# Kernel tuning notes

Hardware: AMD Instinct MI355X
Metric: run time of the kernel (lower is better)

## Reference

```python
import jax, jax.numpy as jnp
import numpy as np

D_MODEL, D_HIDDEN = 1024, 2048
B, L = 4, 4096


def setup_inputs() -> dict:
    key = jax.random.key(0)
    ks = jax.random.split(key, 16)
    r = lambda k, shape, s: s * jax.random.normal(k, shape, dtype=jnp.float32)
    inp = {
        "x": r(ks[0], (B, L, D_MODEL), 1.0),
        # MambaBlock weights (torch Linear stores [out, in]; bias=False for these)
        "w1": r(ks[1], (D_MODEL, D_MODEL), 0.02),
        "w2": r(ks[2], (D_MODEL, D_MODEL), 0.02),
        "w3": r(ks[3], (D_MODEL, D_MODEL), 0.02),
        # depthwise Conv1d: weight [D, 1, 3], bias [D]
        "conv_w": r(ks[4], (D_MODEL, 1, 3), 0.1),
        "conv_b": r(ks[5], (D_MODEL,), 0.02),
        # SSM linears (with bias). Scales keep exp(-delta*A) in (0,1) and
        # the length-L cumprod away from fp32 underflow.
        "A_w": r(ks[6], (D_HIDDEN, D_MODEL), 0.001),
        "A_b": jnp.ones((D_HIDDEN,), jnp.float32),
        "B_w": r(ks[7], (D_HIDDEN, D_MODEL), 0.02),
        "B_b": jnp.zeros((D_HIDDEN,), jnp.float32),
        "C_w": r(ks[8], (D_MODEL, D_HIDDEN), 0.02),
        "C_b": jnp.zeros((D_MODEL,), jnp.float32),
        "D_w": r(ks[9], (D_MODEL, D_MODEL), 0.02),
        "D_b": jnp.zeros((D_MODEL,), jnp.float32),
        "dl_w": r(ks[10], (D_HIDDEN, D_MODEL), 0.001),
        "dl_b": -5.0 * jnp.ones((D_HIDDEN,), jnp.float32),
    }
    return inp


def _lin(x, w, b=None):
    y = jnp.einsum("bld,od->blo", x, w)
    return y if b is None else y + b


def _depthwise_conv(x, conv_w, conv_b):
    # x: [B, L, D] -> torch Conv1d(D, D, k=3, pad=1, groups=D) on [B, D, L]
    lhs = jnp.transpose(x, (0, 2, 1))  # [B, D, L]
    y = jax.lax.conv_general_dilated(
        lhs, conv_w, window_strides=(1,), padding=[(1, 1)],
        dimension_numbers=("NCH", "OIH", "NCH"), feature_group_count=D_MODEL)
    y = y + conv_b[None, :, None]
    return jnp.transpose(y, (0, 2, 1))  # [B, L, D]


def reference(x, w1, w2, w3, conv_w, conv_b, A_w, A_b, B_w, B_b,
              C_w, C_b, D_w, D_b, dl_w, dl_b):
    x = _lin(x, w1)                              # linear1 (no bias)
    x = _depthwise_conv(x, conv_w, conv_b)       # depthwise conv1d
    x = jax.nn.silu(x)
    # SSM
    x_delta = jax.nn.softplus(_lin(x, dl_w, dl_b))   # [B, L, H]
    A_t = _lin(x, A_w, A_b)                          # [B, L, H]
    A_bar = jnp.exp(-x_delta * A_t)                  # [B, L, H]
    B_x = _lin(x, B_w, B_b)                          # [B, L, H]
    A_cum = jnp.cumprod(A_bar, axis=1)               # scan over seq
    h = jnp.cumsum(B_x * A_cum, axis=1)
    ssm_out = _lin(h, C_w, C_b) + _lin(x, D_w, D_b)  # [B, L, D]
    # gated output
    x_res = jax.nn.silu(_lin(ssm_out, w2))
    z = ssm_out * x_res
    out = ssm_out + _lin(z, w3)
    return out
```

## Files before the change

### kernel.cpp

```cpp
#include <hip/hip_runtime.h>
#include <hip/hip_bf16.h>
#include <stdint.h>
#include <math.h>

#define DM 1024
#define DH 2048
#define NB 4
#define SL 4096
#define MT (NB*SL)
#define LC 256
#define NC (SL/LC)

typedef __bf16 bf16;
typedef __attribute__((ext_vector_type(8))) __bf16 bf16x8;
typedef __attribute__((ext_vector_type(4))) __bf16 bf16x4;
typedef __attribute__((ext_vector_type(4))) float f32x4;

struct CvtArgs {
  const float* in[9];
  bf16* out[9];
  int cum[10];
};

__global__ void cvt_all(CvtArgs a) {
  const int total4 = a.cum[9];
  for (int i = blockIdx.x * 256 + threadIdx.x; i < total4; i += gridDim.x * 256) {
    int s = 0;
#pragma unroll 8
    while (i >= a.cum[s + 1]) ++s;
    const int j = i - a.cum[s];
    f32x4 v = *(const f32x4*)(a.in[s] + 4 * (size_t)j);
    bf16x4 o;
#pragma unroll
    for (int k = 0; k < 4; ++k) {
      float x = v[k];
      x = (x == x) ? fminf(fmaxf(x, -65504.f), 65504.f) : 0.f;
      o[k] = (bf16)x;
    }
    *(bf16x4*)(a.out[s] + 4 * (size_t)j) = o;
  }
}


__device__ __forceinline__ void g2lds(const bf16* g, bf16* l) {
  __builtin_amdgcn_global_load_lds((const __attribute__((address_space(1))) void*)g,
                                   (__attribute__((address_space(3))) void*)l,
                                   16, 0, 0);
}

template<int KK>
__device__ __forceinline__ void gemm_pass(const bf16* __restrict__ Abase,
                                          const bf16* __restrict__ Wbase,
                                          bf16* lds_a, bf16* lds_b,
                                          f32x4 (&acc)[4][4],
                                          int wave, int lane,
                                          size_t arow0, size_t brow0) {
  const int wm = wave >> 1, wn = wave & 1;
  const int r_in = lane >> 3;
  const int kc_l = (lane & 7) ^ r_in;
  const int mrow = lane & 15;
  const int kg   = lane >> 4;

  const bf16* pa[4];
  const bf16* pb[4];
#pragma unroll
  for (int iss = 0; iss < 4; ++iss) {
    const int row = (iss * 4 + wave) * 8 + r_in;
    pa[iss] = Abase + (arow0 + row) * (size_t)KK + kc_l * 8;
    pb[iss] = Wbase + (brow0 + row) * (size_t)KK + kc_l * 8;
  }

#pragma unroll 1
  for (int k0 = 0; k0 < KK; k0 += 64) {
    __syncthreads();
#pragma unroll
    for (int iss = 0; iss < 4; ++iss) {
      const int chunk = iss * 4 + wave;
      g2lds(pa[iss], &lds_a[chunk * 512]); pa[iss] += 64;
      g2lds(pb[iss], &lds_b[chunk * 512]); pb[iss] += 64;
    }
    __syncthreads();
#pragma unroll
    for (int ks = 0; ks < 2; ++ks) {
      bf16x8 af[4], bfr[4];
#pragma unroll
      for (int t = 0; t < 4; ++t) {
        const int ra = wm * 64 + t * 16 + mrow;
        const int sa = ra * 8 + ((ks * 4 + kg) ^ (ra & 7));
        af[t] = *(const bf16x8*)&lds_a[sa * 8];
        const int rb = wn * 64 + t * 16 + mrow;
        const int sb = rb * 8 + ((ks * 4 + kg) ^ (rb & 7));
        bfr[t] = *(const bf16x8*)&lds_b[sb * 8];
      }
#pragma unroll
      for (int i = 0; i < 4; ++i)
#pragma unroll
        for (int j = 0; j < 4; ++j)
          acc[i][j] = __builtin_amdgcn_mfma_f32_16x16x32_bf16(af[i], bfr[j], acc[i][j], 0, 0, 0);
    }
  }
}

template<int MODE, bool HAS_BIAS, int N, int K1, int K2>
__global__ __launch_bounds__(256, 4)
void gemm_bt(const bf16* __restrict__ A1, const bf16* __restrict__ W1,
             const float* __restrict__ bias1,
             const bf16* __restrict__ A2, const bf16* __restrict__ W2,
             const float* __restrict__ bias2,
             const void* __restrict__ extra, void* __restrict__ outp) {
  __shared__ __align__(16) char pool[34816];
  bf16* lds_a = (bf16*)pool;
  bf16* lds_b = (bf16*)(pool + 16384);

  const int tid  = threadIdx.x;
  const int wave = tid >> 6;
  const int lane = tid & 63;
  const int wm = wave >> 1, wn = wave & 1;

  constexpr int NBN = N / 128;
  const int nbm8 = (int)(gridDim.y >> 3);
  const int id   = (int)(blockIdx.y * NBN + blockIdx.x);
  const int xcd  = id & 7;
  const unsigned jj = (unsigned)id >> 3;
  const int bm   = xcd * nbm8 + (int)(jj / (unsigned)NBN);
  const int bn   = (int)(jj & (NBN - 1));
  const size_t arow0 = (size_t)bm * 128;
  const size_t brow0 = (size_t)bn * 128;

  f32x4 acc[4][4];
#pragma unroll
  for (int i = 0; i < 4; ++i)
#pragma unroll
    for (int j = 0; j < 4; ++j) acc[i][j] = {0.f, 0.f, 0.f, 0.f};

  gemm_pass<K1>(A1, W1, lds_a, lds_b, acc, wave, lane, arow0, brow0);
  if constexpr (K2 > 0)
    gemm_pass<K2>(A2, W2, lds_a, lds_b, acc, wave, lane, arow0, brow0);

  const int mrow = lane & 15;
  const int kg   = lane >> 4;

  __syncthreads();
  float* eps = (float*)pool + wave * 2176;
  const int rr  = lane >> 3;
  const int cc  = (lane & 7) * 8;
  const int gcol0 = bn * 128 + wn * 64 + cc;
  f32x4 bv0 = {0.f, 0.f, 0.f, 0.f}, bv1 = {0.f, 0.f, 0.f, 0.f};
  if constexpr (HAS_BIAS) {
    bv0 = *(const f32x4*)(bias1 + gcol0);
    bv1 = *(const f32x4*)(bias1 + gcol0 + 4);
  }
  if constexpr (K2 > 0) {
    bv0 += *(const f32x4*)(bias2 + gcol0);
    bv1 += *(const f32x4*)(bias2 + gcol0 + 4);
  }

#pragma unroll
  for (int p = 0; p < 2; ++p) {
#pragma unroll
    for (int ii = 0; ii < 2; ++ii) {
      const int i = p * 2 + ii;
#pragma unroll
      for (int j = 0; j < 4; ++j)
#pragma unroll
        for (int r = 0; r < 4; ++r)
          eps[(ii * 16 + kg * 4 + r) * 68 + j * 16 + mrow] = acc[i][j][r];
    }
#pragma unroll
    for (int rnd = 0; rnd < 4; ++rnd) {
      const int lr   = rnd * 8 + rr;
      const int grow = bm * 128 + wm * 64 + p * 32 + lr;
      f32x4 v0 = *(const f32x4*)&eps[lr * 68 + cc];
      f32x4 v1 = *(const f32x4*)&eps[lr * 68 + cc + 4];
      const size_t off = (size_t)grow * N + gcol0;
      float vv[8];
#pragma unroll
      for (int k = 0; k < 4; ++k) { vv[k] = v0[k] + bv0[k]; vv[4 + k] = v1[k] + bv1[k]; }

      float res[8];
      if constexpr (MODE == 0) {
#pragma unroll
        for (int k = 0; k < 8; ++k) res[k] = vv[k];
      } else if constexpr (MODE == 1) {
        bf16x8 e = *(const bf16x8*)((const bf16*)extra + off);
#pragma unroll
        for (int k = 0; k < 8; ++k) res[k] = vv[k] + (float)e[k];
      } else {
        bf16x8 g = *(const bf16x8*)((const bf16*)extra + off);
#pragma unroll
        for (int k = 0; k < 8; ++k) {
          const float v = vv[k];
          res[k] = (float)g[k] * (v / (1.f + __expf(-v)));
        }
      }

      if constexpr (MODE == 1) {
        f32x4 o0, o1;
#pragma unroll
        for (int k = 0; k < 4; ++k) { o0[k] = res[k]; o1[k] = res[4 + k]; }
        *(f32x4*)((float*)outp + off)     = o0;
        *(f32x4*)((float*)outp + off + 4) = o1;
      } else {
        bf16x8 o;
#pragma unroll
        for (int k = 0; k < 8; ++k) o[k] = (bf16)res[k];
        *(bf16x8*)((bf16*)outp + off) = o;
      }
    }
  }
}

template<int N, int K>
__global__ __launch_bounds__(256, 2)
void gemm_dual(const bf16* __restrict__ A, const bf16* __restrict__ W1,
               const bf16* __restrict__ W2, const float* __restrict__ b1,
               const float* __restrict__ b2, bf16* __restrict__ outp) {
  __shared__ __align__(16) char pool[49152];
  bf16* lds_a  = (bf16*)pool;
  bf16* lds_b1 = (bf16*)(pool + 16384);
  bf16* lds_b2 = (bf16*)(pool + 32768);

  const int tid  = threadIdx.x;
  const int wave = tid >> 6;
  const int lane = tid & 63;
  const int wm = wave >> 1, wn = wave & 1;

  constexpr int NBN = N / 128;
  const int nbm8 = (int)(gridDim.y >> 3);
  const int id   = (int)(blockIdx.y * NBN + blockIdx.x);
  const int xcd  = id & 7;
  const unsigned jj = (unsigned)id >> 3;
  const int bm   = xcd * nbm8 + (int)(jj / (unsigned)NBN);
  const int bn   = (int)(jj & (NBN - 1));
  const size_t arow0 = (size_t)bm * 128;
  const size_t brow0 = (size_t)bn * 128;

  const int r_in = lane >> 3;
  const int kc_l = (lane & 7) ^ r_in;
  const int mrow = lane & 15;
  const int kg   = lane >> 4;

  f32x4 acc1[4][4], acc2[4][4];
#pragma unroll
  for (int i = 0; i < 4; ++i)
#pragma unroll
    for (int j = 0; j < 4; ++j) { acc1[i][j] = {0.f,0.f,0.f,0.f}; acc2[i][j] = {0.f,0.f,0.f,0.f}; }

  const bf16* pa[4]; const bf16* pb1[4]; const bf16* pb2[4];
#pragma unroll
  for (int iss = 0; iss < 4; ++iss) {
    const int row = (iss * 4 + wave) * 8 + r_in;
    pa[iss]  = A  + (arow0 + row) * (size_t)K + kc_l * 8;
    pb1[iss] = W1 + (brow0 + row) * (size_t)K + kc_l * 8;
    pb2[iss] = W2 + (brow0 + row) * (size_t)K + kc_l * 8;
  }

#pragma unroll 1
  for (int k0 = 0; k0 < K; k0 += 64) {
    __syncthreads();
#pragma unroll
    for (int iss = 0; iss < 4; ++iss) {
      const int chunk = iss * 4 + wave;
      g2lds(pa[iss],  &lds_a [chunk * 512]); pa[iss]  += 64;
      g2lds(pb1[iss], &lds_b1[chunk * 512]); pb1[iss] += 64;
      g2lds(pb2[iss], &lds_b2[chunk * 512]); pb2[iss] += 64;
    }
    __syncthreads();
#pragma unroll
    for (int ks = 0; ks < 2; ++ks) {
      bf16x8 af[4], b1f[4], b2f[4];
#pragma unroll
      for (int t = 0; t < 4; ++t) {
        const int ra = wm * 64 + t * 16 + mrow;
        const int sa = ra * 8 + ((ks * 4 + kg) ^ (ra & 7));
        af[t] = *(const bf16x8*)&lds_a[sa * 8];
        const int rb = wn * 64 + t * 16 + mrow;
        const int sb = rb * 8 + ((ks * 4 + kg) ^ (rb & 7));
        b1f[t] = *(const bf16x8*)&lds_b1[sb * 8];
        b2f[t] = *(const bf16x8*)&lds_b2[sb * 8];
      }
#pragma unroll
      for (int i = 0; i < 4; ++i)
#pragma unroll
        for (int j = 0; j < 4; ++j) {
          acc1[i][j] = __builtin_amdgcn_mfma_f32_16x16x32_bf16(af[i], b1f[j], acc1[i][j], 0, 0, 0);
          acc2[i][j] = __builtin_amdgcn_mfma_f32_16x16x32_bf16(af[i], b2f[j], acc2[i][j], 0, 0, 0);
        }
    }
  }

  __syncthreads();
  float* eps1 = (float*)pool + wave * 2176;
  float* eps2 = eps1 + 1088;
  const int rr  = lane >> 3;
  const int cc  = (lane & 7) * 8;
  const int gcol0 = bn * 128 + wn * 64 + cc;
  f32x4 b1v0 = *(const f32x4*)(b1 + gcol0);
  f32x4 b1v1 = *(const f32x4*)(b1 + gcol0 + 4);
  f32x4 b2v0 = *(const f32x4*)(b2 + gcol0);
  f32x4 b2v1 = *(const f32x4*)(b2 + gcol0 + 4);

#pragma unroll
  for (int i = 0; i < 4; ++i) {
#pragma unroll
    for (int j = 0; j < 4; ++j)
#pragma unroll
      for (int r = 0; r < 4; ++r) {
        const int lr = kg * 4 + r;
        eps1[lr * 68 + j * 16 + mrow] = acc1[i][j][r];
        eps2[lr * 68 + j * 16 + mrow] = acc2[i][j][r];
      }
#pragma unroll
    for (int rnd = 0; rnd < 2; ++rnd) {
      const int lr   = rnd * 8 + rr;
      const int grow = bm * 128 + wm * 64 + i * 16 + lr;
      f32x4 u0  = *(const f32x4*)&eps1[lr * 68 + cc];
      f32x4 u1  = *(const f32x4*)&eps1[lr * 68 + cc + 4];
      f32x4 w0  = *(const f32x4*)&eps2[lr * 68 + cc];
      f32x4 w1v = *(const f32x4*)&eps2[lr * 68 + cc + 4];
      const size_t off = (size_t)grow * N + gcol0;
      bf16x8 o;
#pragma unroll
      for (int k = 0; k < 8; ++k) {
        const float dv = (k < 4 ? u0[k] + b1v0[k] : u1[k - 4] + b1v1[k - 4]);
        const float av = (k < 4 ? w0[k] + b2v0[k] : w1v[k - 4] + b2v1[k - 4]);
        const float sp = (dv > 15.f) ? dv : __logf(1.f + __expf(dv));
        o[k] = (bf16)(sp * av);
      }
      *(bf16x8*)(outp + off) = o;
    }
  }
}

__global__ void conv_silu_kernel(const bf16* __restrict__ t1, const float* __restrict__ cw,
                                 const float* __restrict__ cb, bf16* __restrict__ xc) {
  const int gid  = blockIdx.x * 256 + threadIdx.x;
  const int dgrp = gid & (DM / 8 - 1);
  const int bl   = gid >> 7;
  const int l    = bl & (SL - 1);
  const int d0   = dgrp * 8;
  const bf16* p  = t1 + (size_t)bl * DM + d0;
  bf16x8 cc = *(const bf16x8*)p;
  bf16x8 lf, rt;
#pragma unroll
  for (int j = 0; j < 8; ++j) { lf[j] = (bf16)0.f; rt[j] = (bf16)0.f; }
  if (l > 0)      lf = *(const bf16x8*)(p - DM);
  if (l < SL - 1) rt = *(const bf16x8*)(p + DM);
  bf16x8 o;
#pragma unroll
  for (int j = 0; j < 8; ++j) {
    const int d = d0 + j;
    float y = cw[d * 3 + 0] * (float)lf[j] + cw[d * 3 + 1] * (float)cc[j]
            + cw[d * 3 + 2] * (float)rt[j] + cb[d];
    y = y / (1.f + __expf(-y));
    o[j] = (bf16)y;
  }
  *(bf16x8*)(xc + (size_t)bl * DM + d0) = o;
}

__global__ void scan_phase1(bf16* nla_sl, const bf16* __restrict__ bx,
                            float* __restrict__ Lp_tot, float* __restrict__ T_tot) {
  const int g  = blockIdx.x * 256 + threadIdx.x;
  const int ch = g & (DH - 1);
  const int rc = g >> 11;
  const int b  = rc & (NB - 1);
  const int c  = rc >> 2;
  const int bc = b * DH + ch;
  size_t off = ((size_t)(b * SL + c * LC)) * DH + ch;
  float lp = 0.f, S = 0.f;
#pragma unroll 8
  for (int l = 0; l < LC; ++l, off += DH) {
    const float a = (float)nla_sl[off];
    const float x = (float)bx[off];
    lp += a;
    const float e = __expf(-fminf(fmaxf(lp, -80.f), 80.f));
    S = fmaf(x, e, S);
    nla_sl[off] = (bf16)S;
  }
  Lp_tot[c * (NB * DH) + bc] = lp;
  T_tot [c * (NB * DH) + bc] = S;
}

__global__ void scan_phase2(const float* __restrict__ Lp_tot, const float* __restrict__ T_tot,
                            float* __restrict__ lpoff, float* __restrict__ Soff) {
  const int bc = blockIdx.x * 256 + threadIdx.x;
  float lp = 0.f, S = 0.f;
#pragma unroll
  for (int c = 0; c < NC; ++c) {
    lpoff[c * (NB * DH) + bc] = lp;
    Soff [c * (NB * DH) + bc] = S;
    const float e = __expf(-fminf(fmaxf(lp, -80.f), 80.f));
    S  = fmaf(e, T_tot[c * (NB * DH) + bc], S);
    lp += Lp_tot[c * (NB * DH) + bc];
  }
}

__global__ void scan_phase3(const bf16* __restrict__ S_local, bf16* __restrict__ h,
                            const float* __restrict__ lpoff, const float* __restrict__ Soff) {
  const int g  = blockIdx.x * 256 + threadIdx.x;
  const int ch = g & (DH - 1);
  const int rc = g >> 11;
  const int b  = rc & (NB - 1);
  const int c  = rc >> 2;
  const int bc = b * DH + ch;
  const float lo = lpoff[c * (NB * DH) + bc];
  const float so = Soff [c * (NB * DH) + bc];
  const float es = __expf(-fminf(fmaxf(lo, -80.f), 80.f));
  size_t off = ((size_t)(b * SL + c * LC)) * DH + ch;
#pragma unroll 8
  for (int l = 0; l < LC; ++l, off += DH) {
    h[off] = (bf16)fmaf(es, (float)S_local[off], so);
  }
}

extern "C" void kernel_launch(void* const* d_in, const int* in_sizes, int n_in,
                              void* d_out, int out_size, void* d_ws, size_t ws_size,
                              hipStream_t stream) {
  const float* x    = (const float*)d_in[0];
  const float* w1   = (const float*)d_in[1];
  const float* w2   = (const float*)d_in[2];
  const float* w3   = (const float*)d_in[3];
  const float* cw   = (const float*)d_in[4];
  const float* cb   = (const float*)d_in[5];
  const float* A_w  = (const float*)d_in[6];
  const float* A_b  = (const float*)d_in[7];
  const float* B_w  = (const float*)d_in[8];
  const float* B_b  = (const float*)d_in[9];
  const float* C_w  = (const float*)d_in[10];
  const float* C_b  = (const float*)d_in[11];
  const float* D_w  = (const float*)d_in[12];
  const float* D_b  = (const float*)d_in[13];
  const float* dl_w = (const float*)d_in[14];
  const float* dl_b = (const float*)d_in[15];

  const size_t MB = 1048576u;
  char* ws = (char*)d_ws;
  bf16* w1b  = (bf16*)(ws + 0*MB);
  bf16* w2b  = (bf16*)(ws + 2*MB);
  bf16* w3b  = (bf16*)(ws + 4*MB);
  bf16* Dwb  = (bf16*)(ws + 6*MB);
  bf16* Awb  = (bf16*)(ws + 8*MB);
  bf16* Bwb  = (bf16*)(ws + 12*MB);
  bf16* dlwb = (bf16*)(ws + 16*MB);
  bf16* Cwb  = (bf16*)(ws + 20*MB);
  bf16* xc   = (bf16*)(ws + 24*MB);
  bf16* t1   = (bf16*)(ws + 56*MB);
  bf16* z    = t1;
  bf16* xbf  = (bf16*)(ws + 88*MB);
  bf16* bxh  = (bf16*)(ws + 56*MB);
  bf16* nla  = (bf16*)(ws + 120*MB);
  bf16* ssm  = (bf16*)(ws + 120*MB);
  float* Lp_tot = (float*)(ws + 184*MB);
  float* T_tot  = (float*)(ws + 184*MB + 524288u);
  float* lpoff  = (float*)(ws + 185*MB);
  float* Soff   = (float*)(ws + 185*MB + 524288u);
  float* outp = (float*)d_out;

  dim3 blk(256);
  dim3 g1(DM / 128, MT / 128);
  dim3 g2(DH / 128, MT / 128);

  {
    CvtArgs a;
    const float* ins[9]  = {x, w1, w2, w3, D_w, A_w, B_w, dl_w, C_w};
    bf16*        outs[9] = {xbf, w1b, w2b, w3b, Dwb, Awb, Bwb, dlwb, Cwb};
    const int    n4s[9]  = {MT*DM/4, DM*DM/4, DM*DM/4, DM*DM/4, DM*DM/4,
                            DH*DM/4, DH*DM/4, DH*DM/4, DM*DH/4};
    int c = 0;
    a.cum[0] = 0;
    for (int i = 0; i < 9; ++i) { a.in[i] = ins[i]; a.out[i] = outs[i]; c += n4s[i]; a.cum[i+1] = c; }
    cvt_all<<<2048, blk, 0, stream>>>(a);
  }

  gemm_bt<0,false,DM,DM,0><<<g1, blk, 0, stream>>>(xbf, w1b, nullptr,
      nullptr, nullptr, nullptr, nullptr, t1);
  conv_silu_kernel<<<MT * DM / 8 / 256, blk, 0, stream>>>(t1, cw, cb, xc);
  gemm_dual<DH,DM><<<g2, blk, 0, stream>>>(xc, dlwb, Awb, dl_b, A_b, nla);
  gemm_bt<0,true ,DH,DM,0><<<g2, blk, 0, stream>>>(xc, Bwb, B_b,
      nullptr, nullptr, nullptr, nullptr, bxh);
  scan_phase1<<<MT * NC * DH / SL / 256, blk, 0, stream>>>(nla, bxh, Lp_tot, T_tot);
  scan_phase2<<<NB * DH / 256, blk, 0, stream>>>(Lp_tot, T_tot, lpoff, Soff);
  scan_phase3<<<MT * NC * DH / SL / 256, blk, 0, stream>>>(nla, bxh, lpoff, Soff);
  gemm_bt<0,true ,DM,DH,DM><<<g1, blk, 0, stream>>>(bxh, Cwb, C_b,
      xc, Dwb, D_b, nullptr, ssm);
  gemm_bt<2,false,DM,DM,0><<<g1, blk, 0, stream>>>(ssm, w2b, nullptr,
      nullptr, nullptr, nullptr, ssm, z);
  gemm_bt<1,false,DM,DM,0><<<g1, blk, 0, stream>>>(z,   w3b, nullptr,
      nullptr, nullptr, nullptr, ssm, outp);
}
```

Measured before the change: 642.3 us.

## Replace 128x128 GEMM with double-buffered 256x256 eight-wave pipelined GEMM

Swaps the single-buffered 128x128 tile GEMM, which used 4 waves and two syncthreads per K step, for a 256x256 tile kernel with 8 waves. It double-buffers LDS, splits each K step into four phases that interleave global-to-LDS staging with MFMA work, and uses explicit vmcnt waits, barriers and setprio. The intent is to hide load latency and raise data reuse per tile. In exchange it uses 128KB of LDS and needs far more accumulator registers, giving one block per CU, and the grids become smaller: for N=1024 there are only 256 blocks, which may leave CUs underused.

After: 735.5 us. +14.5%, slower.

```diff
diff --git a/kernel.cpp b/kernel.cpp
--- a/kernel.cpp
+++ b/kernel.cpp
@@ -41,110 +41,144 @@
   }
 }
 
-
 __device__ __forceinline__ void g2lds(const bf16* g, bf16* l) {
   __builtin_amdgcn_global_load_lds((const __attribute__((address_space(1))) void*)g,
                                    (__attribute__((address_space(3))) void*)l,
                                    16, 0, 0);
 }
 
-template<int KK>
-__device__ __forceinline__ void gemm_pass(const bf16* __restrict__ Abase,
-                                          const bf16* __restrict__ Wbase,
-                                          bf16* lds_a, bf16* lds_b,
-                                          f32x4 (&acc)[4][4],
-                                          int wave, int lane,
-                                          size_t arow0, size_t brow0) {
-  const int wm = wave >> 1, wn = wave & 1;
+#define G256_PHASE(RH, CH, STAGE, VM)                                         \
+  {                                                                           \
+    bf16x8 af[4][2], bfr[2][2];                                               \
+    _Pragma("unroll")                                                         \
+    for (int rf = 0; rf < 4; ++rf) {                                          \
+      const int ra = wm*128 + ((RH)*4+rf)*16 + mrow;                          \
+      _Pragma("unroll")                                                       \
+      for (int ks = 0; ks < 2; ++ks)                                          \
+        af[rf][ks] = *(const bf16x8*)&lA[(ra*8 + ((ks*4+kg)^(ra&7)))*8];      \
+    }                                                                         \
+    _Pragma("unroll")                                                         \
+    for (int cf = 0; cf < 2; ++cf) {                                          \
+      const int rb = wn*64 + ((CH)*2+cf)*16 + mrow;                           \
+      _Pragma("unroll")                                                       \
+      for (int ks = 0; ks < 2; ++ks)                                          \
+        bfr[cf][ks] = *(const bf16x8*)&lB[(rb*8 + ((ks*4+kg)^(rb&7)))*8];     \
+    }                                                                         \
+    STAGE;                                                                    \
+    __builtin_amdgcn_s_barrier();                                             \
+    __builtin_amdgcn_s_setprio(1);                                            \
+    _Pragma("unroll")                                                         \
+    for (int rf = 0; rf < 4; ++rf)                                            \
+      _Pragma("unroll")                                                       \
+      for (int cf = 0; cf < 2; ++cf)                                          \
+        _Pragma("unroll")                                                     \
+        for (int ks = 0; ks < 2; ++ks)                                        \
+          acc[(RH)*4+rf][(CH)*2+cf] = __builtin_amdgcn_mfma_f32_16x16x32_bf16(\
+              af[rf][ks], bfr[cf][ks], acc[(RH)*4+rf][(CH)*2+cf], 0, 0, 0);   \
+    __builtin_amdgcn_s_setprio(0);                                            \
+    VM;                                                                       \
+    __builtin_amdgcn_s_barrier();                                             \
+  }
+
+template<int MODE, bool HAS_BIAS, int N, int K1, int K2>
+__global__ __launch_bounds__(512, 1)
+void gemm256(const bf16* __restrict__ A1, const bf16* __restrict__ W1,
+             const float* __restrict__ bias1,
+             const bf16* __restrict__ A2, const bf16* __restrict__ W2,
+             const float* __restrict__ bias2,
+             const void* __restrict__ extra, void* __restrict__ outp) {
+  constexpr int NT1 = K1 / 64;
+  constexpr int NT  = (K1 + K2) / 64;
+  __shared__ __align__(16) char pool[131072];
+  bf16* const bA0 = (bf16*)pool;
+  bf16* const bA1 = bA0 + 16384;
+  bf16* const bB0 = bA0 + 32768;
+  bf16* const bB1 = bA0 + 49152;
+
+  const int tid  = threadIdx.x;
+  const int wave = tid >> 6;
+  const int lane = tid & 63;
+  const int wm = wave >> 2, wn = wave & 3;
   const int r_in = lane >> 3;
   const int kc_l = (lane & 7) ^ r_in;
   const int mrow = lane & 15;
   const int kg   = lane >> 4;
 
-  const bf16* pa[4];
-  const bf16* pb[4];
-#pragma unroll
-  for (int iss = 0; iss < 4; ++iss) {
-    const int row = (iss * 4 + wave) * 8 + r_in;
-    pa[iss] = Abase + (arow0 + row) * (size_t)KK + kc_l * 8;
-    pb[iss] = Wbase + (brow0 + row) * (size_t)KK + kc_l * 8;
-  }
-
-#pragma unroll 1
-  for (int k0 = 0; k0 < KK; k0 += 64) {
-    __syncthreads();
-#pragma unroll
-    for (int iss = 0; iss < 4; ++iss) {
-      const int chunk = iss * 4 + wave;
-      g2lds(pa[iss], &lds_a[chunk * 512]); pa[iss] += 64;
-      g2lds(pb[iss], &lds_b[chunk * 512]); pb[iss] += 64;
-    }
-    __syncthreads();
-#pragma unroll
-    for (int ks = 0; ks < 2; ++ks) {
-      bf16x8 af[4], bfr[4];
-#pragma unroll
-      for (int t = 0; t < 4; ++t) {
-        const int ra = wm * 64 + t * 16 + mrow;
-        const int sa = ra * 8 + ((ks * 4 + kg) ^ (ra & 7));
-        af[t] = *(const bf16x8*)&lds_a[sa * 8];
-        const int rb = wn * 64 + t * 16 + mrow;
-        const int sb = rb * 8 + ((ks * 4 + kg) ^ (rb & 7));
-        bfr[t] = *(const bf16x8*)&lds_b[sb * 8];
-      }
-#pragma unroll
-      for (int i = 0; i < 4; ++i)
-#pragma unroll
-        for (int j = 0; j < 4; ++j)
-          acc[i][j] = __builtin_amdgcn_mfma_f32_16x16x32_bf16(af[i], bfr[j], acc[i][j], 0, 0, 0);
-    }
-  }
-}
-
-template<int MODE, bool HAS_BIAS, int N, int K1, int K2>
-__global__ __launch_bounds__(256, 4)
-void gemm_bt(const bf16* __restrict__ A1, const bf16* __restrict__ W1,
-             const float* __restrict__ bias1,
-             const bf16* __restrict__ A2, const bf16* __restrict__ W2,
-             const float* __restrict__ bias2,
-             const void* __restrict__ extra, void* __restrict__ outp) {
-  __shared__ __align__(16) char pool[34816];
-  bf16* lds_a = (bf16*)pool;
-  bf16* lds_b = (bf16*)(pool + 16384);
-
-  const int tid  = threadIdx.x;
-  const int wave = tid >> 6;
-  const int lane = tid & 63;
-  const int wm = wave >> 1, wn = wave & 1;
-
-  constexpr int NBN = N / 128;
+  constexpr int NBN = N / 256;
   const int nbm8 = (int)(gridDim.y >> 3);
   const int id   = (int)(blockIdx.y * NBN + blockIdx.x);
   const int xcd  = id & 7;
   const unsigned jj = (unsigned)id >> 3;
   const int bm   = xcd * nbm8 + (int)(jj / (unsigned)NBN);
   const int bn   = (int)(jj & (NBN - 1));
-  const size_t arow0 = (size_t)bm * 128;
-  const size_t brow0 = (size_t)bn * 128;
-
-  f32x4 acc[4][4];
-#pragma unroll
-  for (int i = 0; i < 4; ++i)
+  const int arow0 = bm * 256;
+  const int brow0 = bn * 256;
+
+  auto stageA = [&](int h, int t, bf16* dst) {
+#pragma unroll
+    for (int j = 0; j < 2; ++j) {
+      const int idx = wave * 2 + j;
+      const int c   = h * 8 + (idx & 7) + ((idx & 8) << 1);
+      const int grow = arow0 + c * 8 + r_in;
+      const bf16* src;
+      if constexpr (K2 > 0) {
+        if (t < NT1) src = A1 + (size_t)grow * K1 + t * 64 + kc_l * 8;
+        else         src = A2 + (size_t)grow * K2 + (t - NT1) * 64 + kc_l * 8;
+      } else {
+        src = A1 + (size_t)grow * K1 + t * 64 + kc_l * 8;
+      }
+      g2lds(src, dst + c * 512);
+    }
+  };
+  auto stageB = [&](int h, int t, bf16* dst) {
+#pragma unroll
+    for (int j = 0; j < 2; ++j) {
+      const int idx = wave * 2 + j;
+      const int c   = ((idx >> 2) << 3) + h * 4 + (idx & 3);
+      const int grow = brow0 + c * 8 + r_in;
+      const bf16* src;
+      if constexpr (K2 > 0) {
+        if (t < NT1) src = W1 + (size_t)grow * K1 + t * 64 + kc_l * 8;
+        else         src = W2 + (size_t)grow * K2 + (t - NT1) * 64 + kc_l * 8;
+      } else {
+        src = W1 + (size_t)grow * K1 + t * 64 + kc_l * 8;
+      }
+      g2lds(src, dst + c * 512);
+    }
+  };
+
+  f32x4 acc[8][4];
+#pragma unroll
+  for (int i = 0; i < 8; ++i)
 #pragma unroll
     for (int j = 0; j < 4; ++j) acc[i][j] = {0.f, 0.f, 0.f, 0.f};
 
-  gemm_pass<K1>(A1, W1, lds_a, lds_b, acc, wave, lane, arow0, brow0);
-  if constexpr (K2 > 0)
-    gemm_pass<K2>(A2, W2, lds_a, lds_b, acc, wave, lane, arow0, brow0);
-
-  const int mrow = lane & 15;
-  const int kg   = lane >> 4;
+  stageA(0, 0, bA0); stageB(0, 0, bB0);
+  stageA(1, 0, bA0); stageB(1, 0, bB0);
+  stageA(0, 1, bA1); stageB(0, 1, bB1);
+  asm volatile("s_waitcnt vmcnt(8)" ::: "memory");
+  __builtin_amdgcn_s_barrier();
+
+#pragma unroll 1
+  for (int k = 0; k < NT; ++k) {
+    const int kb = k & 1;
+    bf16* const lA = kb ? bA1 : bA0;
+    bf16* const lB = kb ? bB1 : bB0;
+    bf16* const oA = kb ? bA0 : bA1;
+    bf16* const oB = kb ? bB0 : bB1;
+    G256_PHASE(0, 0, { if (k + 1 < NT) stageA(1, k + 1, oA); },
+               asm volatile("s_waitcnt vmcnt(6)" ::: "memory"))
+    G256_PHASE(0, 1, { if (k + 1 < NT) stageB(1, k + 1, oB); }, )
+    G256_PHASE(1, 0, { if (k + 2 < NT) stageA(0, k + 2, lA); }, )
+    G256_PHASE(1, 1, { if (k + 2 < NT) stageB(0, k + 2, lB); },
+               asm volatile("s_waitcnt vmcnt(8)" ::: "memory"))
+  }
 
   __syncthreads();
   float* eps = (float*)pool + wave * 2176;
   const int rr  = lane >> 3;
   const int cc  = (lane & 7) * 8;
-  const int gcol0 = bn * 128 + wn * 64 + cc;
+  const int gcol0 = bn * 256 + wn * 64 + cc;
   f32x4 bv0 = {0.f, 0.f, 0.f, 0.f}, bv1 = {0.f, 0.f, 0.f, 0.f};
   if constexpr (HAS_BIAS) {
     bv0 = *(const f32x4*)(bias1 + gcol0);
@@ -156,20 +190,20 @@
   }
 
 #pragma unroll
-  for (int p = 0; p < 2; ++p) {
-#pragma unroll
-    for (int ii = 0; ii < 2; ++ii) {
-      const int i = p * 2 + ii;
-#pragma unroll
-      for (int j = 0; j < 4; ++j)
+  for (int p = 0; p < 4; ++p) {
+#pragma unroll
+    for (int rfp = 0; rfp < 2; ++rfp) {
+      const int rf = p * 2 + rfp;
+#pragma unroll
+      for (int cf = 0; cf < 4; ++cf)
 #pragma unroll
         for (int r = 0; r < 4; ++r)
-          eps[(ii * 16 + kg * 4 + r) * 68 + j * 16 + mrow] = acc[i][j][r];
+          eps[(rfp * 16 + kg * 4 + r) * 68 + cf * 16 + mrow] = acc[rf][cf][r];
     }
 #pragma unroll
     for (int rnd = 0; rnd < 4; ++rnd) {
       const int lr   = rnd * 8 + rr;
-      const int grow = bm * 128 + wm * 64 + p * 32 + lr;
+      const int grow = bm * 256 + wm * 128 + p * 32 + lr;
       f32x4 v0 = *(const f32x4*)&eps[lr * 68 + cc];
       f32x4 v1 = *(const f32x4*)&eps[lr * 68 + cc + 4];
       const size_t off = (size_t)grow * N + gcol0;
@@ -457,7 +491,9 @@
   float* outp = (float*)d_out;
 
   dim3 blk(256);
-  dim3 g1(DM / 128, MT / 128);
+  dim3 blk512(512);
+  dim3 g1_256(DM / 256, MT / 256);
+  dim3 g2_256(DH / 256, MT / 256);
   dim3 g2(DH / 128, MT / 128);
 
   {
@@ -472,19 +508,19 @@
     cvt_all<<<2048, blk, 0, stream>>>(a);
   }
 
-  gemm_bt<0,false,DM,DM,0><<<g1, blk, 0, stream>>>(xbf, w1b, nullptr,
+  gemm256<0,false,DM,DM,0><<<g1_256, blk512, 0, stream>>>(xbf, w1b, nullptr,
       nullptr, nullptr, nullptr, nullptr, t1);
   conv_silu_kernel<<<MT * DM / 8 / 256, blk, 0, stream>>>(t1, cw, cb, xc);
   gemm_dual<DH,DM><<<g2, blk, 0, stream>>>(xc, dlwb, Awb, dl_b, A_b, nla);
-  gemm_bt<0,true ,DH,DM,0><<<g2, blk, 0, stream>>>(xc, Bwb, B_b,
+  gemm256<0,true ,DH,DM,0><<<g2_256, blk512, 0, stream>>>(xc, Bwb, B_b,
       nullptr, nullptr, nullptr, nullptr, bxh);
   scan_phase1<<<MT * NC * DH / SL / 256, blk, 0, stream>>>(nla, bxh, Lp_tot, T_tot);
   scan_phase2<<<NB * DH / 256, blk, 0, stream>>>(Lp_tot, T_tot, lpoff, Soff);
   scan_phase3<<<MT * NC * DH / SL / 256, blk, 0, stream>>>(nla, bxh, lpoff, Soff);
-  gemm_bt<0,true ,DM,DH,DM><<<g1, blk, 0, stream>>>(bxh, Cwb, C_b,
+  gemm256<0,true ,DM,DH,DM><<<g1_256, blk512, 0, stream>>>(bxh, Cwb, C_b,
       xc, Dwb, D_b, nullptr, ssm);
-  gemm_bt<2,false,DM,DM,0><<<g1, blk, 0, stream>>>(ssm, w2b, nullptr,
+  gemm256<2,false,DM,DM,0><<<g1_256, blk512, 0, stream>>>(ssm, w2b, nullptr,
       nullptr, nullptr, nullptr, ssm, z);
-  gemm_bt<1,false,DM,DM,0><<<g1, blk, 0, stream>>>(z,   w3b, nullptr,
+  gemm256<1,false,DM,DM,0><<<g1_256, blk512, 0, stream>>>(z,   w3b, nullptr,
       nullptr, nullptr, nullptr, ssm, outp);
 }
```
